# Performance work log

Hardware: AMD Instinct MI355X
Metric: run time of the kernel (lower is better)

## Reference

```python
import jax, jax.numpy as jnp
import numpy as np
from jax import lax

B, L, C, P = 512, 6, 4, 45

def _conv(x, w, b, pad):
    y = lax.conv_general_dilated(x, w, (1, 1), [(pad, pad), (pad, pad)],
                                 dimension_numbers=('NCHW', 'OIHW', 'NCHW'))
    return y + b[None, :, None, None]

def _maxpool2(x):
    return lax.reduce_window(x, -jnp.inf, lax.max, (1, 1, 2, 2), (1, 1, 2, 2), 'VALID')

def _prelu(x, a):
    return jnp.where(x >= 0, x, a * x)

def setup_inputs() -> dict:
    key = jax.random.key(0)
    ks = jax.random.split(key, 16)
    s = 0.05
    inp = {
        'x': jax.random.normal(ks[0], (B, L, C, P, P), jnp.float32),
        'w0': jax.random.normal(ks[1], (32, C, 5, 5), jnp.float32) * s,
        'b0': jnp.zeros((32,), jnp.float32),
        'w1': jax.random.normal(ks[2], (32, 32, 5, 5), jnp.float32) * s,
        'b1': jnp.zeros((32,), jnp.float32),
        'w2': jax.random.normal(ks[3], (64, 32, 4, 4), jnp.float32) * s,
        'b2': jnp.zeros((64,), jnp.float32),
        'w3': jax.random.normal(ks[4], (64, 64, 3, 3), jnp.float32) * s,
        'b3': jnp.zeros((64,), jnp.float32),
        'a0': jnp.float32(0.25), 'a1': jnp.float32(0.25),
        'a2': jnp.float32(0.25), 'a3': jnp.float32(0.25),
        'fc1_w': jax.random.normal(ks[5], (L, 256, 128), jnp.float32) * s,
        'fc1_b': jnp.zeros((L, 128), jnp.float32),
        'a4': jnp.full((L, 1), 0.25, jnp.float32),
        'fc2_w': jax.random.normal(ks[6], (L, 128, 64), jnp.float32) * s,
        'fc2_b': jnp.zeros((L, 64), jnp.float32),
        'a5': jnp.full((L, 1), 0.25, jnp.float32),
        'fc3_w': jax.random.normal(ks[7], (L, 64, 4), jnp.float32) * s,
        'fc3_b': jnp.zeros((L, 4), jnp.float32),
    }
    return inp

def reference(x, w0, b0, w1, b1, w2, b2, w3, b3, a0, a1, a2, a3,
              fc1_w, fc1_b, a4, fc2_w, fc2_b, a5, fc3_w, fc3_b):
    b, l = x.shape[0], x.shape[1]
    # Conv tower shares weights across landmarks -> fold landmark into batch.
    h = x.reshape(b * l, x.shape[2], P, P)
    h = _maxpool2(_prelu(_conv(h, w0, b0, 1), a0))   # (BL,32,21,21)
    h = _maxpool2(_prelu(_conv(h, w1, b1, 1), a1))   # (BL,32,9,9)
    h = _maxpool2(_prelu(_conv(h, w2, b2, 1), a2))   # (BL,64,4,4)
    h = _prelu(_conv(h, w3, b3, 0), a3)              # (BL,64,2,2)
    h = h.reshape(b, l, 256)
    # Per-landmark FC heads as batched GEMMs.
    h = _prelu(jnp.einsum('bli,lio->blo', h, fc1_w) + fc1_b, a4)
    h = _prelu(jnp.einsum('bli,lio->blo', h, fc2_w) + fc2_b, a5)
    out = jnp.einsum('bli,lio->blo', h, fc3_w) + fc3_b   # (B,L,4)
    return out
```

## Files before the change

### kernel.cpp

```cpp
#include <hip/hip_runtime.h>
#include <stdint.h>

typedef _Float16 f16;
typedef _Float16 half8 __attribute__((ext_vector_type(8)));
typedef _Float16 half4 __attribute__((ext_vector_type(4)));
typedef float floatx16 __attribute__((ext_vector_type(16)));

#define NIMG 3072

#define WS_W0T   0
#define WS_W1T   10240
#define WS_W2T   61440
#define WS_W3T   126976
#define WS_FC1T  200704
#define WS_FC2T  593920
#define WS_FC3T  692224
#define WS_H3F   720896

#define Z16 {0.f,0.f,0.f,0.f,0.f,0.f,0.f,0.f,0.f,0.f,0.f,0.f,0.f,0.f,0.f,0.f}

__global__ __launch_bounds__(256) void k_prep(
    const float* __restrict__ w0, const float* __restrict__ w1, const float* __restrict__ w2,
    const float* __restrict__ w3, const float* __restrict__ fc1w, const float* __restrict__ fc2w,
    const float* __restrict__ fc3w,
    f16* __restrict__ w0t, f16* __restrict__ w1t, f16* __restrict__ w2t, f16* __restrict__ w3t,
    f16* __restrict__ fc1t, f16* __restrict__ fc2t, f16* __restrict__ fc3t)
{
  int stride = gridDim.x * blockDim.x;
  int g0 = blockIdx.x * blockDim.x + threadIdx.x;
  for (int i = g0; i < 5120; i += stride) {
    int j = i & 7, co = (i >> 3) & 31, hf = (i >> 8) & 1, ch = (i >> 9) & 1, ky = i >> 10;
    int k = ch * 16 + hf * 8 + j;
    f16 v = (f16)0.f;
    if (k < 20) { int kx = k >> 2, ci = k & 3; v = (f16)w0[((co * 4 + ci) * 5 + ky) * 5 + kx]; }
    w0t[i] = v;
  }
  for (int i = g0; i < 25600; i += stride) {
    int j = i & 7, co = (i >> 3) & 31, hf = (i >> 8) & 1, ch = (i >> 9) & 1, tap = i >> 10;
    int ci = ch * 16 + hf * 8 + j, ky = tap / 5, kx = tap % 5;
    w1t[i] = (f16)w1[((co * 32 + ci) * 5 + ky) * 5 + kx];
  }
  for (int i = g0; i < 32768; i += stride) {
    int j = i & 7, co = (i >> 3) & 31, hf = (i >> 8) & 1, ct = (i >> 9) & 1, ch = (i >> 10) & 1, tap = i >> 11;
    int ci = ch * 16 + hf * 8 + j, cog = ct * 32 + co, ky = tap >> 2, kx = tap & 3;
    w2t[i] = (f16)w2[((cog * 32 + ci) * 4 + ky) * 4 + kx];
  }
  for (int i = g0; i < 36864; i += stride) {
    int j = i & 7, col = (i >> 3) & 31, hf = (i >> 8) & 1, ct = (i >> 9) & 1, c = i >> 10;
    int k = c * 16 + hf * 8 + j, tap = k >> 6, ci = k & 63, co = ct * 32 + col;
    int ky = tap / 3, kx = tap % 3;
    w3t[i] = (f16)w3[((co * 64 + ci) * 3 + ky) * 3 + kx];
  }
  for (int i = g0; i < 196608; i += stride) {
    int j = i & 7, col = (i >> 3) & 31, hf = (i >> 8) & 1, nt = (i >> 9) & 3, c = (i >> 11) & 15, l = i >> 15;
    int k = c * 16 + hf * 8 + j, o = nt * 32 + col;
    fc1t[i] = (f16)fc1w[(l * 256 + k) * 128 + o];
  }
  for (int i = g0; i < 49152; i += stride) {
    int j = i & 7, col = (i >> 3) & 31, hf = (i >> 8) & 1, nt = (i >> 9) & 1, c = (i >> 10) & 7, l = i >> 13;
    int k = c * 16 + hf * 8 + j, o = nt * 32 + col;
    fc2t[i] = (f16)fc2w[(l * 128 + k) * 64 + o];
  }
  for (int i = g0; i < 12288; i += stride) {
    int j = i & 7, col = (i >> 3) & 31, hf = (i >> 8) & 1, c = (i >> 9) & 3, l = i >> 11;
    int k = c * 16 + hf * 8 + j;
    f16 v = (f16)0.f;
    if (col < 4) v = (f16)fc3w[(l * 64 + k) * 4 + col];
    fc3t[i] = v;
  }
}

__global__ __launch_bounds__(512) void k_conv012(
    const float* __restrict__ x,
    const f16* __restrict__ w0t, const float* __restrict__ b0, const float* __restrict__ a0p,
    const f16* __restrict__ w1t, const float* __restrict__ b1, const float* __restrict__ a1p,
    const f16* __restrict__ w2t, const float* __restrict__ b2, const float* __restrict__ a2p,
    f16* __restrict__ h3f)
{
  __shared__ __align__(16) uint32_t smem_u[19584];
  f16* sh   = (f16*)smem_u;
  f16* s_x  = sh;
  f16* s_h1 = sh + 10528;
  f16* s_h2 = sh + 33408;

  const int n = blockIdx.x, tid = threadIdx.x;
  const int wv = tid >> 6, l = tid & 63;
  const int hf = l >> 5, m = l & 31, dr = m >> 3, dc = m & 7, col = m;
  const float a0 = a0p[0], a1 = a1p[0];
  const float b0c = b0[col], b1c = b1[col];
  const half8* w0t8 = (const half8*)w0t;
  const half8* w1t8 = (const half8*)w1t;
  const half8* w2t8 = (const half8*)w2t;

  {
    uint4 zz = {0u, 0u, 0u, 0u};
    uint4* z = (uint4*)smem_u;
    for (int i = tid; i < 4896; i += 512) z[i] = zz;
  }
  __syncthreads();

  {
    const float* xin = x + n * 8100;
    int idx = tid;
    int y = tid / 45, xx = tid - y * 45, ci = 0;
    #pragma unroll 1
    for (int it = 0; it < 16; ++it) {
      if (idx < 8100) s_x[((y + 1) * 56 + (xx + 1)) * 4 + ci] = (f16)xin[idx];
      idx += 512;
      xx += 17; y += 11;
      if (xx >= 45) { xx -= 45; ++y; }
      if (y >= 45) { y -= 45; ++ci; }
    }
  }
  __syncthreads();

  half8 B0[5][2];
  #pragma unroll
  for (int ky = 0; ky < 5; ++ky)
    #pragma unroll
    for (int ch = 0; ch < 2; ++ch)
      B0[ky][ch] = w0t8[(ky * 2 + ch) * 64 + hf * 32 + col];

  {
    int tr = 0, tc = wv;
    if (tc >= 6) { tc -= 6; tr = 1; }
    #pragma unroll 1
    for (int t = wv; t < 66; t += 8) {
      int r0 = min(tr * 4, 38), cb = tc * 8;
      int rowb = r0 + dr, colb = cb + dc;
      const f16* pA = s_x + (rowb * 56 + colb + 2 * hf) * 4;
      floatx16 acc = Z16;
      #pragma unroll
      for (int ky = 0; ky < 5; ++ky) {
        const f16* p = pA + ky * 224;
        half4 l0  = *(const half4*)(p);
        half4 h0  = *(const half4*)(p + 4);
        half4 l1  = *(const half4*)(p + 16);
        half4 h1v = *(const half4*)(p + 20);
        half8 a0v = __builtin_shufflevector(l0, h0, 0,1,2,3,4,5,6,7);
        half8 a1v = __builtin_shufflevector(l1, h1v, 0,1,2,3,4,5,6,7);
        acc = __builtin_amdgcn_mfma_f32_32x32x16_f16(a0v, B0[ky][0], acc, 0, 0, 0);
        acc = __builtin_amdgcn_mfma_f32_32x32x16_f16(a1v, B0[ky][1], acc, 0, 0, 0);
      }
      #pragma unroll
      for (int pp = 0; pp < 2; ++pp)
        #pragma unroll
        for (int c2 = 0; c2 < 2; ++c2) {
          float v = fmaxf(fmaxf(acc[8*pp + 2*c2], acc[8*pp + 2*c2 + 1]),
                          fmaxf(acc[8*pp + 4 + 2*c2], acc[8*pp + 4 + 2*c2 + 1]));
          v += b0c; v = (v >= 0.f) ? v : a0 * v;
          int pr = (r0 >> 1) + pp, pc = (cb >> 1) + 2 * hf + c2;
          if (pc < 21) s_h1[((pr + 1) * 26 + (pc + 1)) * 40 + col] = (f16)v;
        }
      tc += 2; tr += 1;
      if (tc >= 6) { tc -= 6; ++tr; }
    }
  }
  __syncthreads();

  {
    int t0 = wv * 2;
    int t1 = t0 + 1; if (t1 > 14) t1 = 14;
    int q0 = (t0 * 11) >> 5, q1 = (t1 * 11) >> 5;
    int r0a = min(q0 * 4, 14), cca = min((t0 - 3 * q0) * 8, 14);
    int r0b = min(q1 * 4, 14), ccb = min((t1 - 3 * q1) * 8, 14);
    const f16* pAa = s_h1 + ((r0a + dr) * 26 + cca + dc) * 40 + hf * 8;
    const f16* pAb = s_h1 + ((r0b + dr) * 26 + ccb + dc) * 40 + hf * 8;
    floatx16 accA = Z16;
    floatx16 accB = Z16;
    #pragma unroll 1
    for (int ky = 0; ky < 5; ++ky) {
      const half8* wb = w1t8 + ky * 640 + hf * 32 + col;
      const f16* qa = pAa + ky * 1040;
      const f16* qb = pAb + ky * 1040;
      #pragma unroll
      for (int kx = 0; kx < 5; ++kx) {
        #pragma unroll
        for (int ch = 0; ch < 2; ++ch) {
          half8 b  = wb[kx * 128 + ch * 64];
          half8 aA = *(const half8*)(qa + kx * 40 + ch * 16);
          half8 aB = *(const half8*)(qb + kx * 40 + ch * 16);
          accA = __builtin_amdgcn_mfma_f32_32x32x16_f16(aA, b, accA, 0, 0, 0);
          accB = __builtin_amdgcn_mfma_f32_32x32x16_f16(aB, b, accB, 0, 0, 0);
        }
      }
    }
    #pragma unroll
    for (int tt = 0; tt < 2; ++tt) {
      const floatx16 acc = tt ? accB : accA;
      int r0 = tt ? r0b : r0a, cc = tt ? ccb : cca;
      #pragma unroll
      for (int pp = 0; pp < 2; ++pp)
        #pragma unroll
        for (int c2 = 0; c2 < 2; ++c2) {
          float v = fmaxf(fmaxf(acc[8*pp + 2*c2], acc[8*pp + 2*c2 + 1]),
                          fmaxf(acc[8*pp + 4 + 2*c2], acc[8*pp + 4 + 2*c2 + 1]));
          v += b1c; v = (v >= 0.f) ? v : a1 * v;
          int pr = (r0 >> 1) + pp, pc = (cc >> 1) + 2 * hf + c2;
          if (pc < 9) s_h2[((pr + 1) * 12 + (pc + 1)) * 40 + col] = (f16)v;
        }
    }
  }
  __syncthreads();

  if (wv < 4) {
    const int mt = wv >> 1, ct = wv & 1;
    const float a2 = a2p[0];
    const float b2c = b2[ct * 32 + col];
    const f16* pA = s_h2 + ((mt * 4 + dr) * 12 + dc) * 40 + hf * 8;
    floatx16 acc = Z16;
    #pragma unroll 1
    for (int tap = 0; tap < 16; ++tap) {
      int ky = tap >> 2, kx = tap & 3;
      int aoff = (ky * 12 + kx) * 40;
      #pragma unroll
      for (int ch = 0; ch < 2; ++ch) {
        half8 b  = w2t8[tap * 256 + ch * 128 + ct * 64 + hf * 32 + col];
        half8 av = *(const half8*)(pA + aoff + ch * 16);
        acc = __builtin_amdgcn_mfma_f32_32x32x16_f16(av, b, acc, 0, 0, 0);
      }
    }
    f16* o = h3f + n * 1024;
    #pragma unroll
    for (int pp = 0; pp < 2; ++pp)
      #pragma unroll
      for (int c2 = 0; c2 < 2; ++c2) {
        float v = fmaxf(fmaxf(acc[8*pp + 2*c2], acc[8*pp + 2*c2 + 1]),
                        fmaxf(acc[8*pp + 4 + 2*c2], acc[8*pp + 4 + 2*c2 + 1]));
        v += b2c; v = (v >= 0.f) ? v : a2 * v;
        int pr = mt * 2 + pp, pc = 2 * hf + c2, co = ct * 32 + col;
        o[(pr * 4 + pc) * 64 + co] = (f16)v;
      }
  }
}

__global__ __launch_bounds__(256) void k_tail(
    const f16* __restrict__ h3f,
    const f16* __restrict__ w3t, const float* __restrict__ b3, const float* __restrict__ a3p,
    const f16* __restrict__ fc1t, const float* __restrict__ fc1b, const float* __restrict__ a4,
    const f16* __restrict__ fc2t, const float* __restrict__ fc2b, const float* __restrict__ a5,
    const f16* __restrict__ fc3t, const float* __restrict__ fc3b,
    float* __restrict__ out)
{
  __shared__ __align__(16) f16 s_feat[32 * 264];
  __shared__ __align__(16) f16 s_g1[32 * 136];
  __shared__ __align__(16) f16 s_g2[32 * 72];

  const int lm = blockIdx.x % 6, t = blockIdx.x / 6;
  const int tid = threadIdx.x, wv = tid >> 6, lane = tid & 63;
  const int hf = lane >> 5, col = lane & 31;
  const half8* w3t8  = (const half8*)w3t;
  const half8* fc1t8 = (const half8*)fc1t;
  const half8* fc2t8 = (const half8*)fc2t;
  const half8* fc3t8 = (const half8*)fc3t;

  {
    const int mt = wv;
    const int i_img = mt * 8 + (col >> 2);
    const int pos = col & 3, oy = pos >> 1, ox = pos & 1;
    const int gimg = (t * 32 + i_img) * 6 + lm;
    const f16* Abase = h3f + gimg * 1024 + (oy * 4 + ox) * 64;
    floatx16 acc0 = Z16, acc1 = Z16;
    for (int c = 0; c < 36; ++c) {
      int tap = c >> 2;
      int ky = tap / 3, kx = tap % 3;
      half8 a = *(const half8*)(Abase + (ky * 4 + kx) * 64 + (c & 3) * 16 + hf * 8);
      half8 bb0 = w3t8[((c * 2 + 0) * 2 + hf) * 32 + col];
      half8 bb1 = w3t8[((c * 2 + 1) * 2 + hf) * 32 + col];
      acc0 = __builtin_amdgcn_mfma_f32_32x32x16_f16(a, bb0, acc0, 0, 0, 0);
      acc1 = __builtin_amdgcn_mfma_f32_32x32x16_f16(a, bb1, acc1, 0, 0, 0);
    }
    const float a3 = a3p[0];
    #pragma unroll
    for (int ct = 0; ct < 2; ++ct) {
      const floatx16 acc = ct ? acc1 : acc0;
      const int co = ct * 32 + col;
      const float bb = b3[co];
      #pragma unroll
      for (int q = 0; q < 4; ++q) {
        int ii = mt * 8 + 2 * q + hf;
        half4 w;
        #pragma unroll
        for (int z = 0; z < 4; ++z) {
          float v = acc[q * 4 + z] + bb;
          v = (v >= 0.f) ? v : a3 * v;
          w[z] = (f16)v;
        }
        *(half4*)(s_feat + ii * 264 + co * 4) = w;
      }
    }
  }
  __syncthreads();

  {
    floatx16 g = Z16;
    for (int c = 0; c < 16; ++c) {
      half8 a = *(const half8*)(s_feat + col * 264 + c * 16 + hf * 8);
      half8 b = fc1t8[(((lm * 16 + c) * 4 + wv) * 2 + hf) * 32 + col];
      g = __builtin_amdgcn_mfma_f32_32x32x16_f16(a, b, g, 0, 0, 0);
    }
    const float a4v = a4[lm];
    const float bb = fc1b[lm * 128 + wv * 32 + col];
    #pragma unroll
    for (int reg = 0; reg < 16; ++reg) {
      int r = (reg & 3) + 8 * (reg >> 2) + 4 * hf;
      float v = g[reg] + bb;
      v = (v >= 0.f) ? v : a4v * v;
      s_g1[r * 136 + wv * 32 + col] = (f16)v;
    }
  }
  __syncthreads();

  if (wv < 2) {
    floatx16 g = Z16;
    for (int c = 0; c < 8; ++c) {
      half8 a = *(const half8*)(s_g1 + col * 136 + c * 16 + hf * 8);
      half8 b = fc2t8[(((lm * 8 + c) * 2 + wv) * 2 + hf) * 32 + col];
      g = __builtin_amdgcn_mfma_f32_32x32x16_f16(a, b, g, 0, 0, 0);
    }
    const float a5v = a5[lm];
    const float bb = fc2b[lm * 64 + wv * 32 + col];
    #pragma unroll
    for (int reg = 0; reg < 16; ++reg) {
      int r = (reg & 3) + 8 * (reg >> 2) + 4 * hf;
      float v = g[reg] + bb;
      v = (v >= 0.f) ? v : a5v * v;
      s_g2[r * 72 + wv * 32 + col] = (f16)v;
    }
  }
  __syncthreads();

  if (wv == 0) {
    floatx16 g = Z16;
    for (int c = 0; c < 4; ++c) {
      half8 a = *(const half8*)(s_g2 + col * 72 + c * 16 + hf * 8);
      half8 b = fc3t8[((lm * 4 + c) * 2 + hf) * 32 + col];
      g = __builtin_amdgcn_mfma_f32_32x32x16_f16(a, b, g, 0, 0, 0);
    }
    if (col < 4) {
      const float bb = fc3b[lm * 4 + col];
      #pragma unroll
      for (int reg = 0; reg < 16; ++reg) {
        int r = (reg & 3) + 8 * (reg >> 2) + 4 * hf;
        out[((t * 32 + r) * 6 + lm) * 4 + col] = g[reg] + bb;
      }
    }
  }
}

extern "C" void kernel_launch(void* const* d_in, const int* in_sizes, int n_in,
                              void* d_out, int out_size, void* d_ws, size_t ws_size,
                              hipStream_t stream) {
  const float* x    = (const float*)d_in[0];
  const float* w0   = (const float*)d_in[1];
  const float* b0   = (const float*)d_in[2];
  const float* w1   = (const float*)d_in[3];
  const float* b1   = (const float*)d_in[4];
  const float* w2   = (const float*)d_in[5];
  const float* b2   = (const float*)d_in[6];
  const float* w3   = (const float*)d_in[7];
  const float* b3   = (const float*)d_in[8];
  const float* a0   = (const float*)d_in[9];
  const float* a1   = (const float*)d_in[10];
  const float* a2   = (const float*)d_in[11];
  const float* a3   = (const float*)d_in[12];
  const float* fc1w = (const float*)d_in[13];
  const float* fc1b = (const float*)d_in[14];
  const float* a4   = (const float*)d_in[15];
  const float* fc2w = (const float*)d_in[16];
  const float* fc2b = (const float*)d_in[17];
  const float* a5   = (const float*)d_in[18];
  const float* fc3w = (const float*)d_in[19];
  const float* fc3b = (const float*)d_in[20];
  float* out = (float*)d_out;

  char* ws = (char*)d_ws;
  f16* w0t  = (f16*)(ws + WS_W0T);
  f16* w1t  = (f16*)(ws + WS_W1T);
  f16* w2t  = (f16*)(ws + WS_W2T);
  f16* w3t  = (f16*)(ws + WS_W3T);
  f16* fc1t = (f16*)(ws + WS_FC1T);
  f16* fc2t = (f16*)(ws + WS_FC2T);
  f16* fc3t = (f16*)(ws + WS_FC3T);
  f16* h3f  = (f16*)(ws + WS_H3F);

  k_prep   <<<128, 256, 0, stream>>>(w0, w1, w2, w3, fc1w, fc2w, fc3w,
                                     w0t, w1t, w2t, w3t, fc1t, fc2t, fc3t);
  k_conv012<<<NIMG, 512, 0, stream>>>(x, w0t, b0, a0, w1t, b1, a1, w2t, b2, a2, h3f);
  k_tail   <<<96, 256, 0, stream>>>(h3f, w3t, b3, a3, fc1t, fc1b, a4,
                                    fc2t, fc2b, a5, fc3t, fc3b, out);
}
```

Baseline: 363.1 us.

## Shrink LDS footprint by staging input in two halves and aliasing buffers

Measured after the change: 520.6 us. 1.43x slower.

```diff
diff --git a/kernel.cpp b/kernel.cpp
--- a/kernel.cpp
+++ b/kernel.cpp
@@ -77,11 +77,11 @@
     const f16* __restrict__ w2t, const float* __restrict__ b2, const float* __restrict__ a2p,
     f16* __restrict__ h3f)
 {
-  __shared__ __align__(16) uint32_t smem_u[19584];
+  __shared__ __align__(16) uint32_t smem_u[13432];
   f16* sh   = (f16*)smem_u;
-  f16* s_x  = sh;
-  f16* s_h1 = sh + 10528;
-  f16* s_h2 = sh + 33408;
+  f16* s_xh = sh;
+  f16* s_h1 = sh + 6272;
+  f16* s_h2 = sh;
 
   const int n = blockIdx.x, tid = threadIdx.x;
   const int wv = tid >> 6, l = tid & 63;
@@ -95,22 +95,15 @@
   {
     uint4 zz = {0u, 0u, 0u, 0u};
     uint4* z = (uint4*)smem_u;
-    for (int i = tid; i < 4896; i += 512) z[i] = zz;
-  }
-  __syncthreads();
-
-  {
-    const float* xin = x + n * 8100;
-    int idx = tid;
-    int y = tid / 45, xx = tid - y * 45, ci = 0;
-    #pragma unroll 1
-    for (int it = 0; it < 16; ++it) {
-      if (idx < 8100) s_x[((y + 1) * 56 + (xx + 1)) * 4 + ci] = (f16)xin[idx];
-      idx += 512;
-      xx += 17; y += 11;
-      if (xx >= 45) { xx -= 45; ++y; }
-      if (y >= 45) { y -= 45; ++ci; }
-    }
+    for (int i = tid; i < 3358; i += 512) z[i] = zz;
+  }
+  __syncthreads();
+
+  const float* xin = x + n * 8100;
+  for (int i = tid; i < 4860; i += 512) {
+    int ci = i / 1215, rem = i - ci * 1215;
+    int yy = rem / 45, xx = rem - yy * 45;
+    s_xh[((yy + 1) * 56 + (xx + 1)) * 4 + ci] = (f16)xin[ci * 2025 + rem];
   }
   __syncthreads();
 
@@ -121,85 +114,115 @@
     for (int ch = 0; ch < 2; ++ch)
       B0[ky][ch] = w0t8[(ky * 2 + ch) * 64 + hf * 32 + col];
 
-  {
-    int tr = 0, tc = wv;
-    if (tc >= 6) { tc -= 6; tr = 1; }
-    #pragma unroll 1
-    for (int t = wv; t < 66; t += 8) {
-      int r0 = min(tr * 4, 38), cb = tc * 8;
-      int rowb = r0 + dr, colb = cb + dc;
-      const f16* pA = s_x + (rowb * 56 + colb + 2 * hf) * 4;
-      floatx16 acc = Z16;
-      #pragma unroll
-      for (int ky = 0; ky < 5; ++ky) {
-        const f16* p = pA + ky * 224;
-        half4 l0  = *(const half4*)(p);
-        half4 h0  = *(const half4*)(p + 4);
-        half4 l1  = *(const half4*)(p + 16);
-        half4 h1v = *(const half4*)(p + 20);
-        half8 a0v = __builtin_shufflevector(l0, h0, 0,1,2,3,4,5,6,7);
-        half8 a1v = __builtin_shufflevector(l1, h1v, 0,1,2,3,4,5,6,7);
-        acc = __builtin_amdgcn_mfma_f32_32x32x16_f16(a0v, B0[ky][0], acc, 0, 0, 0);
-        acc = __builtin_amdgcn_mfma_f32_32x32x16_f16(a1v, B0[ky][1], acc, 0, 0, 0);
-      }
-      #pragma unroll
-      for (int pp = 0; pp < 2; ++pp)
-        #pragma unroll
-        for (int c2 = 0; c2 < 2; ++c2) {
-          float v = fmaxf(fmaxf(acc[8*pp + 2*c2], acc[8*pp + 2*c2 + 1]),
-                          fmaxf(acc[8*pp + 4 + 2*c2], acc[8*pp + 4 + 2*c2 + 1]));
-          v += b0c; v = (v >= 0.f) ? v : a0 * v;
-          int pr = (r0 >> 1) + pp, pc = (cb >> 1) + 2 * hf + c2;
-          if (pc < 21) s_h1[((pr + 1) * 26 + (pc + 1)) * 40 + col] = (f16)v;
-        }
-      tc += 2; tr += 1;
-      if (tc >= 6) { tc -= 6; ++tr; }
-    }
-  }
-  __syncthreads();
-
-  {
-    int t0 = wv * 2;
-    int t1 = t0 + 1; if (t1 > 14) t1 = 14;
-    int q0 = (t0 * 11) >> 5, q1 = (t1 * 11) >> 5;
-    int r0a = min(q0 * 4, 14), cca = min((t0 - 3 * q0) * 8, 14);
-    int r0b = min(q1 * 4, 14), ccb = min((t1 - 3 * q1) * 8, 14);
-    const f16* pAa = s_h1 + ((r0a + dr) * 26 + cca + dc) * 40 + hf * 8;
-    const f16* pAb = s_h1 + ((r0b + dr) * 26 + ccb + dc) * 40 + hf * 8;
-    floatx16 accA = Z16;
-    floatx16 accB = Z16;
-    #pragma unroll 1
+  for (int t = wv; t < 36; t += 8) {
+    int r0 = (t / 6) * 4, cb = (t % 6) * 8;
+    const f16* pA = s_xh + ((r0 + dr) * 56 + cb + dc + 2 * hf) * 4;
+    floatx16 acc = Z16;
+    #pragma unroll
     for (int ky = 0; ky < 5; ++ky) {
-      const half8* wb = w1t8 + ky * 640 + hf * 32 + col;
-      const f16* qa = pAa + ky * 1040;
-      const f16* qb = pAb + ky * 1040;
-      #pragma unroll
-      for (int kx = 0; kx < 5; ++kx) {
-        #pragma unroll
-        for (int ch = 0; ch < 2; ++ch) {
-          half8 b  = wb[kx * 128 + ch * 64];
-          half8 aA = *(const half8*)(qa + kx * 40 + ch * 16);
-          half8 aB = *(const half8*)(qb + kx * 40 + ch * 16);
-          accA = __builtin_amdgcn_mfma_f32_32x32x16_f16(aA, b, accA, 0, 0, 0);
-          accB = __builtin_amdgcn_mfma_f32_32x32x16_f16(aB, b, accB, 0, 0, 0);
-        }
-      }
-    }
-    #pragma unroll
-    for (int tt = 0; tt < 2; ++tt) {
-      const floatx16 acc = tt ? accB : accA;
-      int r0 = tt ? r0b : r0a, cc = tt ? ccb : cca;
-      #pragma unroll
-      for (int pp = 0; pp < 2; ++pp)
-        #pragma unroll
-        for (int c2 = 0; c2 < 2; ++c2) {
-          float v = fmaxf(fmaxf(acc[8*pp + 2*c2], acc[8*pp + 2*c2 + 1]),
-                          fmaxf(acc[8*pp + 4 + 2*c2], acc[8*pp + 4 + 2*c2 + 1]));
-          v += b1c; v = (v >= 0.f) ? v : a1 * v;
-          int pr = (r0 >> 1) + pp, pc = (cc >> 1) + 2 * hf + c2;
-          if (pc < 9) s_h2[((pr + 1) * 12 + (pc + 1)) * 40 + col] = (f16)v;
-        }
-    }
+      const f16* p = pA + ky * 224;
+      half4 l0  = *(const half4*)(p);
+      half4 h0  = *(const half4*)(p + 4);
+      half4 l1  = *(const half4*)(p + 16);
+      half4 h1v = *(const half4*)(p + 20);
+      half8 a0v = __builtin_shufflevector(l0, h0, 0,1,2,3,4,5,6,7);
+      half8 a1v = __builtin_shufflevector(l1, h1v, 0,1,2,3,4,5,6,7);
+      acc = __builtin_amdgcn_mfma_f32_32x32x16_f16(a0v, B0[ky][0], acc, 0, 0, 0);
+      acc = __builtin_amdgcn_mfma_f32_32x32x16_f16(a1v, B0[ky][1], acc, 0, 0, 0);
+    }
+    #pragma unroll
+    for (int pp = 0; pp < 2; ++pp)
+      #pragma unroll
+      for (int c2 = 0; c2 < 2; ++c2) {
+        float v = fmaxf(fmaxf(acc[8*pp + 2*c2], acc[8*pp + 2*c2 + 1]),
+                        fmaxf(acc[8*pp + 4 + 2*c2], acc[8*pp + 4 + 2*c2 + 1]));
+        v += b0c; v = (v >= 0.f) ? v : a0 * v;
+        int pr = (r0 >> 1) + pp, pc = (cb >> 1) + 2 * hf + c2;
+        if (pc < 21) s_h1[((pr + 1) * 26 + (pc + 1)) * 36 + col] = (f16)v;
+      }
+  }
+  __syncthreads();
+
+  for (int i = tid; i < 3960; i += 512) {
+    int ci = i / 990, rem = i - ci * 990;
+    int yy = rem / 45, xx = rem - yy * 45;
+    s_xh[(yy * 56 + (xx + 1)) * 4 + ci] = (f16)xin[ci * 2025 + (yy + 23) * 45 + xx];
+  }
+  __syncthreads();
+
+  for (int t = 36 + wv; t < 66; t += 8) {
+    int q = (t - 36) / 6, rr = (t - 36) - q * 6;
+    int r0 = min(24 + q * 4, 38), cb = rr * 8;
+    const f16* pA = s_xh + ((r0 - 24 + dr) * 56 + cb + dc + 2 * hf) * 4;
+    floatx16 acc = Z16;
+    #pragma unroll
+    for (int ky = 0; ky < 5; ++ky) {
+      const f16* p = pA + ky * 224;
+      half4 l0  = *(const half4*)(p);
+      half4 h0  = *(const half4*)(p + 4);
+      half4 l1  = *(const half4*)(p + 16);
+      half4 h1v = *(const half4*)(p + 20);
+      half8 a0v = __builtin_shufflevector(l0, h0, 0,1,2,3,4,5,6,7);
+      half8 a1v = __builtin_shufflevector(l1, h1v, 0,1,2,3,4,5,6,7);
+      acc = __builtin_amdgcn_mfma_f32_32x32x16_f16(a0v, B0[ky][0], acc, 0, 0, 0);
+      acc = __builtin_amdgcn_mfma_f32_32x32x16_f16(a1v, B0[ky][1], acc, 0, 0, 0);
+    }
+    #pragma unroll
+    for (int pp = 0; pp < 2; ++pp)
+      #pragma unroll
+      for (int c2 = 0; c2 < 2; ++c2) {
+        float v = fmaxf(fmaxf(acc[8*pp + 2*c2], acc[8*pp + 2*c2 + 1]),
+                        fmaxf(acc[8*pp + 4 + 2*c2], acc[8*pp + 4 + 2*c2 + 1]));
+        v += b0c; v = (v >= 0.f) ? v : a0 * v;
+        int pr = (r0 >> 1) + pp, pc = (cb >> 1) + 2 * hf + c2;
+        if (pc < 21) s_h1[((pr + 1) * 26 + (pc + 1)) * 36 + col] = (f16)v;
+      }
+  }
+  __syncthreads();
+
+  for (int i = tid; i < 2880; i += 512) smem_u[i] = 0u;
+  __syncthreads();
+
+  const int r0lut1[5] = {0, 4, 8, 12, 14};
+  const int cclut[3]  = {0, 8, 14};
+  int t0 = wv * 2;
+  int t1 = t0 + 1; if (t1 > 14) t1 = 14;
+  int r0a = r0lut1[t0 / 3], cca = cclut[t0 % 3];
+  int r0b = r0lut1[t1 / 3], ccb = cclut[t1 % 3];
+  const f16* pAa = s_h1 + ((r0a + dr) * 26 + cca + dc) * 36 + hf * 8;
+  const f16* pAb = s_h1 + ((r0b + dr) * 26 + ccb + dc) * 36 + hf * 8;
+  floatx16 accA = Z16;
+  floatx16 accB = Z16;
+  for (int ky = 0; ky < 5; ++ky) {
+    const half8* wb = w1t8 + ky * 640 + hf * 32 + col;
+    const f16* qa = pAa + ky * 936;
+    const f16* qb = pAb + ky * 936;
+    #pragma unroll
+    for (int kx = 0; kx < 5; ++kx) {
+      #pragma unroll
+      for (int ch = 0; ch < 2; ++ch) {
+        half8 b  = wb[kx * 128 + ch * 64];
+        half8 aA = *(const half8*)(qa + kx * 36 + ch * 16);
+        half8 aB = *(const half8*)(qb + kx * 36 + ch * 16);
+        accA = __builtin_amdgcn_mfma_f32_32x32x16_f16(aA, b, accA, 0, 0, 0);
+        accB = __builtin_amdgcn_mfma_f32_32x32x16_f16(aB, b, accB, 0, 0, 0);
+      }
+    }
+  }
+  #pragma unroll
+  for (int tt = 0; tt < 2; ++tt) {
+    const floatx16 acc = tt ? accB : accA;
+    int r0 = tt ? r0b : r0a, cc = tt ? ccb : cca;
+    #pragma unroll
+    for (int pp = 0; pp < 2; ++pp)
+      #pragma unroll
+      for (int c2 = 0; c2 < 2; ++c2) {
+        float v = fmaxf(fmaxf(acc[8*pp + 2*c2], acc[8*pp + 2*c2 + 1]),
+                        fmaxf(acc[8*pp + 4 + 2*c2], acc[8*pp + 4 + 2*c2 + 1]));
+        v += b1c; v = (v >= 0.f) ? v : a1 * v;
+        int pr = (r0 >> 1) + pp, pc = (cc >> 1) + 2 * hf + c2;
+        if (pc < 9) s_h2[((pr + 1) * 12 + (pc + 1)) * 40 + col] = (f16)v;
+      }
   }
   __syncthreads();
 
@@ -209,7 +232,6 @@
     const float b2c = b2[ct * 32 + col];
     const f16* pA = s_h2 + ((mt * 4 + dr) * 12 + dc) * 40 + hf * 8;
     floatx16 acc = Z16;
-    #pragma unroll 1
     for (int tap = 0; tap < 16; ++tap) {
       int ky = tap >> 2, kx = tap & 3;
       int aoff = (ky * 12 + kx) * 40;
```
